# Kernel tuning notes

Hardware: AMD Instinct MI355X
Metric: run time of the kernel (lower is better)

## Reference

```python
import jax, jax.numpy as jnp
import numpy as np

N_NODES = 100000
N_EDGES = 1600000
FEAT = 64
HIDDEN = 64
NUM_GRAPHS = 64


def gcn_conv(x, row, col, norm, W, b, n_nodes):
    # x: [N, in], W: [in, out]; PyG GCNConv: transform, then normalized scatter-add, then bias
    xw = x @ W                                   # [N, out]
    msgs = xw[row] * norm[:, None]               # [E+N, out]
    out = jax.ops.segment_sum(msgs, col, num_segments=n_nodes)
    return out + b


def _norm_and_loops(edge_index, n_nodes):
    # add self loops and compute symmetric normalization deg^-1/2 * deg^-1/2
    loop = jnp.arange(n_nodes, dtype=edge_index.dtype)
    row = jnp.concatenate([edge_index[0], loop])  # sources
    col = jnp.concatenate([edge_index[1], loop])  # targets
    ew = jnp.ones(row.shape[0], dtype=jnp.float32)
    deg = jax.ops.segment_sum(ew, col, num_segments=n_nodes)
    dinv = jnp.where(deg > 0, jax.lax.rsqrt(jnp.maximum(deg, 1.0)), 0.0)
    norm = dinv[row] * dinv[col]
    return row, col, norm


def setup_inputs() -> dict:
    key = jax.random.key(0)
    ks = jax.random.split(key, 10)
    x = jax.random.normal(ks[0], (N_NODES, FEAT), dtype=jnp.float32)
    edge_index = jax.random.randint(ks[1], (2, N_EDGES), 0, N_NODES, dtype=jnp.int64 if jax.config.jax_enable_x64 else jnp.int32)
    batch = jnp.sort(jax.random.randint(ks[2], (N_NODES,), 0, NUM_GRAPHS, dtype=edge_index.dtype))
    def xavier(k, fan_in, fan_out):
        lim = np.sqrt(6.0 / (fan_in + fan_out))
        return jax.random.uniform(k, (fan_in, fan_out), minval=-lim, maxval=lim, dtype=jnp.float32)
    W1 = xavier(ks[3], FEAT, HIDDEN)
    W2 = xavier(ks[4], HIDDEN, HIDDEN)
    W3 = xavier(ks[5], HIDDEN, HIDDEN)
    b1 = jnp.zeros((HIDDEN,), jnp.float32)
    b2 = jnp.zeros((HIDDEN,), jnp.float32)
    b3 = jnp.zeros((HIDDEN,), jnp.float32)
    return {"x": x, "edge_index": edge_index, "batch": batch,
            "W1": W1, "b1": b1, "W2": W2, "b2": b2, "W3": W3, "b3": b3}


def reference(x, edge_index, batch, W1, b1, W2, b2, W3, b3):
    n_nodes = x.shape[0]
    row, col, norm = _norm_and_loops(edge_index, n_nodes)
    xs = []
    h = x
    for W, b in ((W1, b1), (W2, b2), (W3, b3)):
        h = gcn_conv(h, row, col, norm, W, b, n_nodes)
        h = jax.nn.relu(h)
        xs.append(h)
    # global_add_pool per layer, then concat along features -> [num_graphs, 3*hidden]
    pooled = [jax.ops.segment_sum(h, batch, num_segments=NUM_GRAPHS) for h in xs]
    return jnp.concatenate(pooled, axis=1)
```

## Files before the change

kernel.cpp:

```cpp
#include <hip/hip_runtime.h>


#define F 64
#define CAP 48
#define NRANGE 8

typedef __attribute__((ext_vector_type(8))) short short8x;
typedef __attribute__((ext_vector_type(8))) unsigned short ushort8x;
typedef __attribute__((ext_vector_type(4))) float f32x4;

static inline size_t alignup(size_t x, size_t a) { return (x + a - 1) & ~(a - 1); }

__device__ __forceinline__ ushort f2bf(float f) {
    unsigned u = __builtin_bit_cast(unsigned, f);
    unsigned r = (u + 0x7fffu + ((u >> 16) & 1u)) >> 16;
    return (ushort)r;
}
__device__ __forceinline__ float bf2f(ushort v) {
    return __builtin_bit_cast(float, ((unsigned)v) << 16);
}

__global__ __launch_bounds__(256) void k_build(const int* __restrict__ rowv,
                                               const int* __restrict__ colv,
                                               int* __restrict__ cnt,
                                               int* __restrict__ csr,
                                               int E, int rsize) {
    int r = blockIdx.x & (NRANGE - 1);
    int e4 = (blockIdx.x >> 3) * 256 + threadIdx.x;
    int lo = r * rsize;
    int hiEx = lo + rsize;
    int E4 = E >> 2;
    if (e4 < E4) {
        int4 c = ((const int4*)colv)[e4];
        int4 s = ((const int4*)rowv)[e4];
        int p;
        if (c.x >= lo && c.x < hiEx) {
            p = atomicAdd(&cnt[c.x], 1);
            if (p < CAP) csr[(size_t)c.x * CAP + p] = s.x;
        }
        if (c.y >= lo && c.y < hiEx) {
            p = atomicAdd(&cnt[c.y], 1);
            if (p < CAP) csr[(size_t)c.y * CAP + p] = s.y;
        }
        if (c.z >= lo && c.z < hiEx) {
            p = atomicAdd(&cnt[c.z], 1);
            if (p < CAP) csr[(size_t)c.z * CAP + p] = s.z;
        }
        if (c.w >= lo && c.w < hiEx) {
            p = atomicAdd(&cnt[c.w], 1);
            if (p < CAP) csr[(size_t)c.w * CAP + p] = s.w;
        }
    }
    int tail = E & 3;
    if (r == 0 && (int)blockIdx.x < NRANGE && (int)threadIdx.x < tail) {
        int e = (E4 << 2) + threadIdx.x;
        int c = colv[e], s = rowv[e];
        int p = atomicAdd(&cnt[c], 1);
        if (p < CAP) csr[(size_t)c * CAP + p] = s;
    }
}

__global__ __launch_bounds__(256) void k_prepx(const float* __restrict__ x,
                                               ushort* __restrict__ xbf, long n4) {
    long i = (long)blockIdx.x * 256 + threadIdx.x;
    if (i < n4) {
        float4 v = ((const float4*)x)[i];
        ushort4 u;
        u.x = f2bf(v.x); u.y = f2bf(v.y); u.z = f2bf(v.z); u.w = f2bf(v.w);
        ((ushort4*)xbf)[i] = u;
    }
}

__global__ __launch_bounds__(256) void k_prepw(const float* __restrict__ W0,
                                               const float* __restrict__ W1,
                                               const float* __restrict__ W2,
                                               ushort* __restrict__ wt) {
    const float* W = (blockIdx.x == 0) ? W0 : (blockIdx.x == 1) ? W1 : W2;
    ushort* o = wt + (size_t)blockIdx.x * F * F;
    for (int i = threadIdx.x; i < F * F; i += 256) {
        int k = i >> 6, c = i & 63;
        o[c * F + k] = f2bf(W[i]);
    }
}

__global__ __launch_bounds__(256) void k_gemm(const ushort* __restrict__ Hbf,
                                              const ushort* __restrict__ WT,
                                              const int* __restrict__ cnt,
                                              ushort* __restrict__ XW, int n) {
    __shared__ ushort hl[64][72];
    __shared__ ushort wl[64][72];
    int rowBase = blockIdx.x * 64;
    for (int i = threadIdx.x; i < 1024; i += 256) {
        int idx = i & 511;
        int row = idx >> 3, cb = (idx & 7) << 3;
        if (i < 512) {
            int gr = rowBase + row;
            short8x v = {0, 0, 0, 0, 0, 0, 0, 0};
            if (gr < n) v = *(const short8x*)(Hbf + (size_t)gr * F + cb);
            *(short8x*)&hl[row][cb] = v;
        } else {
            *(short8x*)&wl[row][cb] = *(const short8x*)(WT + row * F + cb);
        }
    }
    __syncthreads();

    int lane = threadIdx.x & 63;
    int w = threadIdx.x >> 6;
    int l15 = lane & 15, l4 = lane >> 4;

    short8x a0 = *(const short8x*)&hl[w * 16 + l15][l4 * 8];
    short8x a1 = *(const short8x*)&hl[w * 16 + l15][32 + l4 * 8];

    f32x4 acc[4];
#pragma unroll
    for (int ct = 0; ct < 4; ++ct) {
        acc[ct] = (f32x4){0.f, 0.f, 0.f, 0.f};
        short8x b0 = *(const short8x*)&wl[ct * 16 + l15][l4 * 8];
        short8x b1 = *(const short8x*)&wl[ct * 16 + l15][32 + l4 * 8];
        acc[ct] = __builtin_amdgcn_mfma_f32_16x16x32_bf16(a0, b0, acc[ct], 0, 0, 0);
        acc[ct] = __builtin_amdgcn_mfma_f32_16x16x32_bf16(a1, b1, acc[ct], 0, 0, 0);
    }

#pragma unroll
    for (int r = 0; r < 4; ++r) {
        int gr = rowBase + w * 16 + l4 * 4 + r;
        if (gr < n) {
            float sc = rsqrtf((float)cnt[gr] + 1.0f);
#pragma unroll
            for (int ct = 0; ct < 4; ++ct) {
                XW[(size_t)gr * F + ct * 16 + l15] = f2bf(acc[ct][r] * sc);
            }
        }
    }
}

__global__ __launch_bounds__(256) void k_gather(const ushort* __restrict__ XW,
                                                const int* __restrict__ cnt,
                                                const int* __restrict__ csr,
                                                const float* __restrict__ bias,
                                                ushort* __restrict__ h,
                                                int n) {
    int lane = threadIdx.x & 63;
    int q = lane >> 3, s = lane & 7;
    int wave = blockIdx.x * (blockDim.x >> 6) + (threadIdx.x >> 6);
    int node = wave * 8 + q;
    if (node >= n) return;

    float4 bv0 = ((const float4*)bias)[s * 2];
    float4 bv1 = ((const float4*)bias)[s * 2 + 1];

    int deg = cnt[node];
    int dmax = min(deg, CAP);
    const int* cr = csr + (size_t)node * CAP;
    const ushort8x* rows = (const ushort8x*)XW;

    float sum[8];
    {
        ushort8x v = rows[(size_t)node * 8 + s];
#pragma unroll
        for (int i = 0; i < 8; ++i) sum[i] = bf2f(v[i]);
    }
    int j = 0;
    for (; j + 4 <= dmax; j += 4) {
        int4 a = *(const int4*)(cr + j);
        ushort8x v0 = rows[(size_t)a.x * 8 + s];
        ushort8x v1 = rows[(size_t)a.y * 8 + s];
        ushort8x v2 = rows[(size_t)a.z * 8 + s];
        ushort8x v3 = rows[(size_t)a.w * 8 + s];
#pragma unroll
        for (int i = 0; i < 8; ++i)
            sum[i] += (bf2f(v0[i]) + bf2f(v1[i])) + (bf2f(v2[i]) + bf2f(v3[i]));
    }
    for (; j < dmax; ++j) {
        ushort8x v = rows[(size_t)cr[j] * 8 + s];
#pragma unroll
        for (int i = 0; i < 8; ++i) sum[i] += bf2f(v[i]);
    }

    float sc = rsqrtf((float)deg + 1.0f);
    ushort8x o;
    o[0] = f2bf(fmaxf(fmaf(sum[0], sc, bv0.x), 0.f));
    o[1] = f2bf(fmaxf(fmaf(sum[1], sc, bv0.y), 0.f));
    o[2] = f2bf(fmaxf(fmaf(sum[2], sc, bv0.z), 0.f));
    o[3] = f2bf(fmaxf(fmaf(sum[3], sc, bv0.w), 0.f));
    o[4] = f2bf(fmaxf(fmaf(sum[4], sc, bv1.x), 0.f));
    o[5] = f2bf(fmaxf(fmaf(sum[5], sc, bv1.y), 0.f));
    o[6] = f2bf(fmaxf(fmaf(sum[6], sc, bv1.z), 0.f));
    o[7] = f2bf(fmaxf(fmaf(sum[7], sc, bv1.w), 0.f));
    ((ushort8x*)h)[(size_t)node * 8 + s] = o;
}

__global__ __launch_bounds__(256) void k_pool(const ushort* __restrict__ h,
                                              const int* __restrict__ batch,
                                              float* __restrict__ out,
                                              int layerOff, int n) {
    __shared__ int se[2];
    __shared__ float part[4][F];
    int g = blockIdx.x;
    if (threadIdx.x == 0) {
        int lo = 0, hi = n;
        while (lo < hi) { int mid = (lo + hi) >> 1; if (batch[mid] < g) lo = mid + 1; else hi = mid; }
        se[0] = lo;
        hi = n;
        while (lo < hi) { int mid = (lo + hi) >> 1; if (batch[mid] < g + 1) lo = mid + 1; else hi = mid; }
        se[1] = lo;
    }
    __syncthreads();
    int start = se[0], end = se[1];
    int f = threadIdx.x & 63;
    int w = threadIdx.x >> 6;
    float s0 = 0.f, s1 = 0.f, s2 = 0.f, s3 = 0.f;
    int node = start + w;
    for (; node + 12 < end; node += 16) {
        s0 += bf2f(h[(size_t)node * F + f]);
        s1 += bf2f(h[(size_t)(node + 4) * F + f]);
        s2 += bf2f(h[(size_t)(node + 8) * F + f]);
        s3 += bf2f(h[(size_t)(node + 12) * F + f]);
    }
    for (; node < end; node += 4) s0 += bf2f(h[(size_t)node * F + f]);
    part[w][f] = (s0 + s1) + (s2 + s3);
    __syncthreads();
    if (threadIdx.x < F) {
        float t = part[0][f] + part[1][f] + part[2][f] + part[3][f];
        out[g * (3 * F) + layerOff + f] = t;
    }
}

extern "C" void kernel_launch(void* const* d_in, const int* in_sizes, int n_in,
                              void* d_out, int out_size, void* d_ws, size_t ws_size,
                              hipStream_t stream) {
    const float* x = (const float*)d_in[0];
    const int* edge = (const int*)d_in[1];
    const int* batch = (const int*)d_in[2];
    const float* Ws[3] = {(const float*)d_in[3], (const float*)d_in[5], (const float*)d_in[7]};
    const float* bs[3] = {(const float*)d_in[4], (const float*)d_in[6], (const float*)d_in[8]};
    float* out = (float*)d_out;

    const int N = in_sizes[0] / F;
    const int E = in_sizes[1] / 2;
    const int* rowv = edge;
    const int* colv = edge + E;

    char* ws = (char*)d_ws;
    size_t off = 0;
    int*    cnt = (int*)(ws + off);    off = alignup(off + (size_t)N * 4, 256);
    int*    csr = (int*)(ws + off);    off = alignup(off + (size_t)N * CAP * 4, 256);
    ushort* xw  = (ushort*)(ws + off); off = alignup(off + (size_t)N * F * 2, 256);
    ushort* h   = (ushort*)(ws + off); off = alignup(off + (size_t)N * F * 2, 256);
    ushort* xbf = (ushort*)(ws + off); off = alignup(off + (size_t)N * F * 2, 256);
    ushort* wt  = (ushort*)(ws + off); off = alignup(off + (size_t)3 * F * F * 2, 256);
    (void)ws_size;

    hipMemsetAsync(cnt, 0, (size_t)N * 4, stream);

    const int rsize = (N + NRANGE - 1) / NRANGE;
    const int chunks = ((E >> 2) + 255) / 256;
    k_build<<<chunks * NRANGE, 256, 0, stream>>>(rowv, colv, cnt, csr, E, rsize);

    const long n4 = ((long)N * F) / 4;
    k_prepx<<<(int)((n4 + 255) / 256), 256, 0, stream>>>(x, xbf, n4);
    k_prepw<<<3, 256, 0, stream>>>(Ws[0], Ws[1], Ws[2], wt);

    const int gemmBlocks = (N + 63) / 64;
    const int gatherWaves = (N + 7) / 8;
    const int gatherBlocks = (gatherWaves + 3) / 4;

    for (int l = 0; l < 3; ++l) {
        const ushort* Hin = (l == 0) ? xbf : h;
        k_gemm<<<gemmBlocks, 256, 0, stream>>>(Hin, wt + (size_t)l * F * F, cnt, xw, N);
        k_gather<<<gatherBlocks, 256, 0, stream>>>(xw, cnt, csr, bs[l], h, N);
        k_pool<<<64, 256, 0, stream>>>(h, batch, out, l * F, N);
    }
}
```

Measured before the change: 327.3 us.

## Fuse global add pooling into gather kernel via shared-memory bins and atomics

Removes the separate pooling kernel: each gather block accumulates its 32 nodes' post-ReLU outputs into per-graph shared-memory bins, then atomically adds the bins into the output. The last layer no longer writes h to global memory, and the output is zeroed with a memset first. This removes one launch per layer and a re-read of h, at the cost of LDS atomics, a block-wide zeroing and sync, and about 3125 blocks issuing global atomics to only 64 output rows. The pooled sums now use fp32 values instead of bf16-rounded h, and summation order changes.

```diff
diff --git a/kernel.cpp b/kernel.cpp
--- a/kernel.cpp
+++ b/kernel.cpp
@@ -138,91 +138,90 @@
                                                 const int* __restrict__ cnt,
                                                 const int* __restrict__ csr,
                                                 const float* __restrict__ bias,
+                                                const int* __restrict__ batch,
                                                 ushort* __restrict__ h,
-                                                int n) {
+                                                float* __restrict__ out,
+                                                int layerOff, int n, int writeH) {
+    __shared__ float bins[32][F];
+    __shared__ int binfo[2];
+    for (int i = threadIdx.x; i < 32 * F; i += 256) ((float*)bins)[i] = 0.f;
+    int blockStart = blockIdx.x * 32;
+    if (threadIdx.x == 0) {
+        int b0 = batch[min(blockStart, n - 1)];
+        int bl = batch[min(blockStart + 31, n - 1)];
+        binfo[0] = b0;
+        binfo[1] = bl - b0;
+    }
+    __syncthreads();
+
     int lane = threadIdx.x & 63;
     int q = lane >> 3, s = lane & 7;
-    int wave = blockIdx.x * (blockDim.x >> 6) + (threadIdx.x >> 6);
-    int node = wave * 8 + q;
-    if (node >= n) return;
-
-    float4 bv0 = ((const float4*)bias)[s * 2];
-    float4 bv1 = ((const float4*)bias)[s * 2 + 1];
-
-    int deg = cnt[node];
-    int dmax = min(deg, CAP);
-    const int* cr = csr + (size_t)node * CAP;
-    const ushort8x* rows = (const ushort8x*)XW;
-
-    float sum[8];
-    {
-        ushort8x v = rows[(size_t)node * 8 + s];
-#pragma unroll
-        for (int i = 0; i < 8; ++i) sum[i] = bf2f(v[i]);
-    }
-    int j = 0;
-    for (; j + 4 <= dmax; j += 4) {
-        int4 a = *(const int4*)(cr + j);
-        ushort8x v0 = rows[(size_t)a.x * 8 + s];
-        ushort8x v1 = rows[(size_t)a.y * 8 + s];
-        ushort8x v2 = rows[(size_t)a.z * 8 + s];
-        ushort8x v3 = rows[(size_t)a.w * 8 + s];
-#pragma unroll
-        for (int i = 0; i < 8; ++i)
-            sum[i] += (bf2f(v0[i]) + bf2f(v1[i])) + (bf2f(v2[i]) + bf2f(v3[i]));
-    }
-    for (; j < dmax; ++j) {
-        ushort8x v = rows[(size_t)cr[j] * 8 + s];
-#pragma unroll
-        for (int i = 0; i < 8; ++i) sum[i] += bf2f(v[i]);
-    }
-
-    float sc = rsqrtf((float)deg + 1.0f);
-    ushort8x o;
-    o[0] = f2bf(fmaxf(fmaf(sum[0], sc, bv0.x), 0.f));
-    o[1] = f2bf(fmaxf(fmaf(sum[1], sc, bv0.y), 0.f));
-    o[2] = f2bf(fmaxf(fmaf(sum[2], sc, bv0.z), 0.f));
-    o[3] = f2bf(fmaxf(fmaf(sum[3], sc, bv0.w), 0.f));
-    o[4] = f2bf(fmaxf(fmaf(sum[4], sc, bv1.x), 0.f));
-    o[5] = f2bf(fmaxf(fmaf(sum[5], sc, bv1.y), 0.f));
-    o[6] = f2bf(fmaxf(fmaf(sum[6], sc, bv1.z), 0.f));
-    o[7] = f2bf(fmaxf(fmaf(sum[7], sc, bv1.w), 0.f));
-    ((ushort8x*)h)[(size_t)node * 8 + s] = o;
-}
-
-__global__ __launch_bounds__(256) void k_pool(const ushort* __restrict__ h,
-                                              const int* __restrict__ batch,
-                                              float* __restrict__ out,
-                                              int layerOff, int n) {
-    __shared__ int se[2];
-    __shared__ float part[4][F];
-    int g = blockIdx.x;
-    if (threadIdx.x == 0) {
-        int lo = 0, hi = n;
-        while (lo < hi) { int mid = (lo + hi) >> 1; if (batch[mid] < g) lo = mid + 1; else hi = mid; }
-        se[0] = lo;
-        hi = n;
-        while (lo < hi) { int mid = (lo + hi) >> 1; if (batch[mid] < g + 1) lo = mid + 1; else hi = mid; }
-        se[1] = lo;
+    int wave = threadIdx.x >> 6;
+    int node = blockStart + wave * 8 + q;
+
+    if (node < n) {
+        float4 bv0 = ((const float4*)bias)[s * 2];
+        float4 bv1 = ((const float4*)bias)[s * 2 + 1];
+
+        int deg = cnt[node];
+        int dmax = min(deg, CAP);
+        const int* cr = csr + (size_t)node * CAP;
+        const ushort8x* rows = (const ushort8x*)XW;
+
+        float sum[8];
+        {
+            ushort8x v = rows[(size_t)node * 8 + s];
+#pragma unroll
+            for (int i = 0; i < 8; ++i) sum[i] = bf2f(v[i]);
+        }
+        int j = 0;
+        for (; j + 4 <= dmax; j += 4) {
+            int4 a = *(const int4*)(cr + j);
+            ushort8x v0 = rows[(size_t)a.x * 8 + s];
+            ushort8x v1 = rows[(size_t)a.y * 8 + s];
+            ushort8x v2 = rows[(size_t)a.z * 8 + s];
+            ushort8x v3 = rows[(size_t)a.w * 8 + s];
+#pragma unroll
+            for (int i = 0; i < 8; ++i)
+                sum[i] += (bf2f(v0[i]) + bf2f(v1[i])) + (bf2f(v2[i]) + bf2f(v3[i]));
+        }
+        for (; j < dmax; ++j) {
+            ushort8x v = rows[(size_t)cr[j] * 8 + s];
+#pragma unroll
+            for (int i = 0; i < 8; ++i) sum[i] += bf2f(v[i]);
+        }
+
+        float sc = rsqrtf((float)deg + 1.0f);
+        float val[8];
+        val[0] = fmaxf(fmaf(sum[0], sc, bv0.x), 0.f);
+        val[1] = fmaxf(fmaf(sum[1], sc, bv0.y), 0.f);
+        val[2] = fmaxf(fmaf(sum[2], sc, bv0.z), 0.f);
+        val[3] = fmaxf(fmaf(sum[3], sc, bv0.w), 0.f);
+        val[4] = fmaxf(fmaf(sum[4], sc, bv1.x), 0.f);
+        val[5] = fmaxf(fmaf(sum[5], sc, bv1.y), 0.f);
+        val[6] = fmaxf(fmaf(sum[6], sc, bv1.z), 0.f);
+        val[7] = fmaxf(fmaf(sum[7], sc, bv1.w), 0.f);
+
+        if (writeH) {
+            ushort8x o;
+#pragma unroll
+            for (int i = 0; i < 8; ++i) o[i] = f2bf(val[i]);
+            ((ushort8x*)h)[(size_t)node * 8 + s] = o;
+        }
+
+        int k = batch[node] - binfo[0];
+        float* bin = &bins[k][s * 8];
+#pragma unroll
+        for (int i = 0; i < 8; ++i) atomicAdd(&bin[i], val[i]);
     }
     __syncthreads();
-    int start = se[0], end = se[1];
-    int f = threadIdx.x & 63;
-    int w = threadIdx.x >> 6;
-    float s0 = 0.f, s1 = 0.f, s2 = 0.f, s3 = 0.f;
-    int node = start + w;
-    for (; node + 12 < end; node += 16) {
-        s0 += bf2f(h[(size_t)node * F + f]);
-        s1 += bf2f(h[(size_t)(node + 4) * F + f]);
-        s2 += bf2f(h[(size_t)(node + 8) * F + f]);
-        s3 += bf2f(h[(size_t)(node + 12) * F + f]);
-    }
-    for (; node < end; node += 4) s0 += bf2f(h[(size_t)node * F + f]);
-    part[w][f] = (s0 + s1) + (s2 + s3);
-    __syncthreads();
-    if (threadIdx.x < F) {
-        float t = part[0][f] + part[1][f] + part[2][f] + part[3][f];
-        out[g * (3 * F) + layerOff + f] = t;
+
+    int b0 = binfo[0], bspan = binfo[1];
+    for (int k = 0; k <= bspan; ++k) {
+        if (threadIdx.x < F) {
+            atomicAdd(&out[(b0 + k) * (3 * F) + layerOff + threadIdx.x],
+                      bins[k][threadIdx.x]);
+        }
     }
 }
 
@@ -251,6 +250,7 @@
     ushort* wt  = (ushort*)(ws + off); off = alignup(off + (size_t)3 * F * F * 2, 256);
     (void)ws_size;
 
+    hipMemsetAsync(out, 0, (size_t)out_size * sizeof(float), stream);
     hipMemsetAsync(cnt, 0, (size_t)N * 4, stream);
 
     const int rsize = (N + NRANGE - 1) / NRANGE;
@@ -262,13 +262,12 @@
     k_prepw<<<3, 256, 0, stream>>>(Ws[0], Ws[1], Ws[2], wt);
 
     const int gemmBlocks = (N + 63) / 64;
-    const int gatherWaves = (N + 7) / 8;
-    const int gatherBlocks = (gatherWaves + 3) / 4;
+    const int gatherBlocks = (N + 31) / 32;
 
     for (int l = 0; l < 3; ++l) {
         const ushort* Hin = (l == 0) ? xbf : h;
         k_gemm<<<gemmBlocks, 256, 0, stream>>>(Hin, wt + (size_t)l * F * F, cnt, xw, N);
-        k_gather<<<gatherBlocks, 256, 0, stream>>>(xw, cnt, csr, bs[l], h, N);
-        k_pool<<<64, 256, 0, stream>>>(h, batch, out, l * F, N);
-    }
-}
+        k_gather<<<gatherBlocks, 256, 0, stream>>>(xw, cnt, csr, bs[l], batch, h, out,
+                                                   l * F, N, (l < 2) ? 1 : 0);
+    }
+}
```

Result: faster. 318.5 us (-2.7%).
